# Performance work log

Measured on AMD Instinct MI355X. Metric: run time of the kernel, lower is better.

Reference implementation:

```python
import jax, jax.numpy as jnp
import numpy as np
import math

B, N, D, H = 4, 2048, 1024, 16
DH = D // H  # dim per head
OUT = 1024

def setup_inputs() -> dict:
    key0 = jax.random.key(0)
    ks = jax.random.split(key0, 12)
    s = 1.0 / math.sqrt(D)
    return {
        "key": jax.random.normal(ks[0], (B, N, D), jnp.float32),
        "value": jax.random.normal(ks[1], (B, N, D), jnp.float32),
        "query": jax.random.normal(ks[2], (B, N, D), jnp.float32),
        "Wk": jax.random.normal(ks[3], (D, D), jnp.float32) * s,
        "bk": jax.random.normal(ks[4], (D,), jnp.float32) * 0.01,
        "Wv": jax.random.normal(ks[5], (D, D), jnp.float32) * s,
        "bv": jax.random.normal(ks[6], (D,), jnp.float32) * 0.01,
        "Wq": jax.random.normal(ks[7], (D, D), jnp.float32) * s,
        "bq": jax.random.normal(ks[8], (D,), jnp.float32) * 0.01,
        "Wo": jax.random.normal(ks[9], (D, OUT), jnp.float32) * s,
        "bo": jax.random.normal(ks[10], (OUT,), jnp.float32) * 0.01,
    }

def reference(key, value, query, Wk, bk, Wv, bv, Wq, bq, Wo, bo):
    scale = math.sqrt(DH)
    k = (key @ Wk + bk).reshape(B, N, H, DH).transpose(0, 2, 1, 3)    # [B,H,N,DH]
    v = (value @ Wv + bv).reshape(B, N, H, DH).transpose(0, 2, 1, 3)
    q = ((query @ Wq + bq) / scale).reshape(B, N, H, DH).transpose(0, 2, 1, 3)
    scores = jnp.einsum('bhqd,bhkd->bhqk', q, k).astype(jnp.float32)  # [B,H,N,N]
    attn = jax.nn.softmax(scores, axis=-1).astype(q.dtype)
    # dropout p=0.0 (eval / identity)
    ctx = jnp.einsum('bhqk,bhkd->bhqd', attn, v)                      # [B,H,N,DH]
    ctx = ctx.transpose(0, 2, 1, 3).reshape(B, N, D)
    out = ctx @ Wo + bo                                               # [B,N,OUT]
    return out
```

## Files before the change

### kernel.cpp

```cpp
#include <hip/hip_runtime.h>
#include <hip/hip_bf16.h>
#include <stdint.h>

#define BB 4
#define NN 2048
#define DD 1024
#define HH 16
#define DHH 64
#define MM (BB*NN)

typedef unsigned short u16;
typedef unsigned int u32;
typedef __bf16 bf16x8_t __attribute__((ext_vector_type(8)));
typedef float f32x4_t __attribute__((ext_vector_type(4)));
typedef float f32x16_t __attribute__((ext_vector_type(16)));

__device__ inline u16 f2b(float f) {
    __hip_bfloat16 h = __float2bfloat16(f);
    return *(u16*)&h;
}

__device__ inline u32 pack2(float lo, float hi) {
    return (u32)f2b(lo) | ((u32)f2b(hi) << 16);
}

__device__ inline void gload16(const void* g, void* l) {
    __builtin_amdgcn_global_load_lds(
        (const __attribute__((address_space(1))) void*)g,
        (__attribute__((address_space(3))) void*)l, 16, 0, 0);
}

__global__ void cvt_kernel(const float* __restrict__ in, u16* __restrict__ out) {
    int i = (blockIdx.x * 256 + threadIdx.x) * 4;
    float4 v = *(const float4*)(in + i);
    ushort4 o;
    o.x = f2b(v.x); o.y = f2b(v.y); o.z = f2b(v.z); o.w = f2b(v.w);
    *(ushort4*)(out + i) = o;
}

__global__ void wtrans_kernel(const float* __restrict__ W0, const float* __restrict__ W1,
                              const float* __restrict__ W2, const float* __restrict__ W3,
                              u16* __restrict__ out_base) {
    int z = blockIdx.z;
    const float* W = (z == 0) ? W0 : (z == 1) ? W1 : (z == 2) ? W2 : W3;
    u16* o = out_base + (size_t)z * DD * DD;
    __shared__ float tile[64][65];
    int t = threadIdx.x;
    int r0 = t >> 6;
    int c = t & 63;
    int kb = blockIdx.x, nb = blockIdx.y;
#pragma unroll
    for (int i = 0; i < 16; ++i) {
        int r = i * 4 + r0;
        tile[r][c] = W[(size_t)(kb * 64 + r) * DD + nb * 64 + c];
    }
    __syncthreads();
#pragma unroll
    for (int i = 0; i < 16; ++i) {
        int r = i * 4 + r0;
        o[(size_t)(nb * 64 + r) * DD + kb * 64 + c] = f2b(tile[c][r]);
    }
}

__global__ void vtrans_kernel(const u16* __restrict__ in, u16* __restrict__ out) {
    __shared__ u16 tile[64][65];
    const int t = threadIdx.x;
    const int r0 = t >> 6;
    const int c = t & 63;
    const int nt = blockIdx.x;
    const int bh = blockIdx.y;
    const int b = bh >> 4, h = bh & 15;
    const u16* src = in + ((size_t)(b * 2048 + nt * 64)) * DD + h * 64;
#pragma unroll
    for (int i = 0; i < 16; ++i) {
        int r = i * 4 + r0;
        tile[r][c] = src[(size_t)r * DD + c];
    }
    __syncthreads();
    u16* dst = out + ((size_t)bh * 64) * NN + nt * 64;
#pragma unroll
    for (int i = 0; i < 16; ++i) {
        int r = i * 4 + r0;
        dst[(size_t)r * NN + c] = tile[c][r];
    }
}

template<int OUT_F32>
__global__ __launch_bounds__(256, 2)
void gemm_bt(const u16* __restrict__ A, const u16* __restrict__ Bt,
             const float* __restrict__ bias, void* __restrict__ Cout, float scale) {
    __shared__ u16 As[128 * 64];
    __shared__ u16 Bs[128 * 64];
    const int t = threadIdx.x;
    const int w = t >> 6, l = t & 63;
    const int wm = w >> 1, wn = w & 1;
    const int g = l >> 4, c = l & 15;
    const int bm = blockIdx.x, bn = blockIdx.y;

    const f32x4_t vzero = {0.f, 0.f, 0.f, 0.f};
    f32x4_t acc[4][4];
#pragma unroll
    for (int m = 0; m < 4; ++m)
#pragma unroll
        for (int n = 0; n < 4; ++n) acc[m][n] = vzero;

    const int srow = l >> 3;
    const int scol = ((l & 7) ^ srow) << 3;
    const int sa = (l & 7) << 4;

    for (int ks = 0; ks < 16; ++ks) {
#pragma unroll
        for (int i = 0; i < 4; ++i) {
            int chunk = w * 4 + i;
            int row = chunk * 8 + srow;
            const u16* ga = A + (size_t)(bm * 128 + row) * DD + ks * 64 + scol;
            gload16(ga, As + chunk * 512);
            const u16* gb = Bt + (size_t)(bn * 128 + row) * DD + ks * 64 + scol;
            gload16(gb, Bs + chunk * 512);
        }
        __syncthreads();

        bf16x8_t af[4][2], bfr[4][2];
#pragma unroll
        for (int m = 0; m < 4; ++m) {
            int rowa = wm * 64 + m * 16 + c;
#pragma unroll
            for (int kk = 0; kk < 2; ++kk)
                af[m][kk] = *(const bf16x8_t*)&As[rowa * 64 + (((kk * 64 + g * 16) ^ sa) >> 1)];
        }
#pragma unroll
        for (int n = 0; n < 4; ++n) {
            int rowb = wn * 64 + n * 16 + c;
#pragma unroll
            for (int kk = 0; kk < 2; ++kk)
                bfr[n][kk] = *(const bf16x8_t*)&Bs[rowb * 64 + (((kk * 64 + g * 16) ^ sa) >> 1)];
        }
#pragma unroll
        for (int kk = 0; kk < 2; ++kk)
#pragma unroll
            for (int m = 0; m < 4; ++m)
#pragma unroll
                for (int n = 0; n < 4; ++n)
                    acc[m][n] = __builtin_amdgcn_mfma_f32_16x16x32_bf16(
                        af[m][kk], bfr[n][kk], acc[m][n], 0, 0, 0);
        __syncthreads();
    }

#pragma unroll
    for (int n = 0; n < 4; ++n) {
        int col = bn * 128 + wn * 64 + n * 16 + c;
        float bv = bias[col];
#pragma unroll
        for (int m = 0; m < 4; ++m) {
            int row = bm * 128 + wm * 64 + m * 16 + g * 4;
#pragma unroll
            for (int j = 0; j < 4; ++j) {
                float v = (acc[m][n][j] + bv) * scale;
                if (OUT_F32)
                    ((float*)Cout)[(size_t)(row + j) * DD + col] = v;
                else
                    ((u16*)Cout)[(size_t)(row + j) * DD + col] = f2b(v);
            }
        }
    }
}

__global__ __launch_bounds__(256, 2)
void attn32_kernel(const u16* __restrict__ qb, const u16* __restrict__ kb,
                   const u16* __restrict__ vt, u16* __restrict__ ctx) {
    __shared__ u16 Kt[2][64 * 64];
    __shared__ u16 Vs[2][64 * 64];
    const int t = threadIdx.x;
    const int w = t >> 6, l = t & 63;
    const int hl = l >> 5, l31 = l & 31, l7 = l & 7, l3 = l >> 3;

    const int f = blockIdx.y * 16 + blockIdx.x;
    const int wg = (f & 7) * 128 + (f >> 3);
    const int qt = wg & 15, bh = wg >> 4;
    const int b = bh >> 4, h = bh & 15;
    const int hoff = h * DHH;
    const size_t kv0 = (size_t)b * NN;
    const size_t vt0 = (size_t)bh * DHH;

    const size_t qrow = (size_t)(b * NN + qt * 128 + w * 32 + l31);
    bf16x8_t qf[4];
#pragma unroll
    for (int dks = 0; dks < 4; ++dks)
        qf[dks] = *(const bf16x8_t*)&qb[qrow * DD + hoff + dks * 16 + hl * 8];

    f32x16_t accO[2];
#pragma unroll
    for (int dt = 0; dt < 2; ++dt)
#pragma unroll
        for (int r = 0; r < 16; ++r) accO[dt][r] = 0.f;
    float lacc[16];
#pragma unroll
    for (int r = 0; r < 16; ++r) lacc[r] = 0.f;

#define STAGE_K(kt_, buf_)                                                   \
    do {                                                                     \
        _Pragma("unroll")                                                    \
        for (int i_ = 0; i_ < 2; ++i_) {                                     \
            int ch_ = w + i_ * 4;                                            \
            int r_ = ch_ * 8 + l3;                                           \
            int rr_ = (r_ >> 2) & 3;                                         \
            int pr_ = (rr_ == 1 || rr_ == 2) ? (r_ ^ 12) : r_;               \
            gload16(kb + (kv0 + (kt_) * 64 + pr_) * DD + hoff +              \
                        ((l7 ^ l3) << 3),                                    \
                    &Kt[buf_][ch_ * 512]);                                   \
        }                                                                    \
    } while (0)
#define STAGE_V(kt_, buf_)                                                   \
    do {                                                                     \
        _Pragma("unroll")                                                    \
        for (int i_ = 0; i_ < 2; ++i_) {                                     \
            int ch_ = w + i_ * 4;                                            \
            int r_ = ch_ * 8 + l3;                                           \
            gload16(vt + (vt0 + r_) * NN + (kt_) * 64 + ((l7 ^ l3) << 3),    \
                    &Vs[buf_][ch_ * 512]);                                   \
        }                                                                    \
    } while (0)

    STAGE_K(0, 0);
    STAGE_V(0, 0);
    __syncthreads();

    for (int kt = 0; kt < NN / 64; ++kt) {
        const int cur = kt & 1;
        if (kt < NN / 64 - 1) {
            STAGE_K(kt + 1, cur ^ 1);
            STAGE_V(kt + 1, cur ^ 1);
        }

        const char* Kc = (const char*)Kt[cur];
        f32x16_t accS[2];
        __builtin_amdgcn_s_setprio(1);
#pragma unroll
        for (int kt32 = 0; kt32 < 2; ++kt32) {
#pragma unroll
            for (int r = 0; r < 16; ++r) accS[kt32][r] = 0.f;
#pragma unroll
            for (int dks = 0; dks < 4; ++dks) {
                bf16x8_t kf = *(const bf16x8_t*)(Kc + (kt32 * 32 + l31) * 128 +
                                                 ((dks * 32 + hl * 16) ^ (l7 << 4)));
                accS[kt32] = __builtin_amdgcn_mfma_f32_32x32x16_bf16(
                    kf, qf[dks], accS[kt32], 0, 0, 0);
            }
        }
        __builtin_amdgcn_s_setprio(0);

#pragma unroll
        for (int r = 0; r < 16; ++r) {
            float p0 = exp2f(accS[0][r]);
            float p1 = exp2f(accS[1][r]);
            accS[0][r] = p0;
            accS[1][r] = p1;
            lacc[r] += p0 + p1;
        }

        const char* Vc = (const char*)Vs[cur];
        __builtin_amdgcn_s_setprio(1);
#pragma unroll
        for (int pm = 0; pm < 4; ++pm) {
            const int kt32 = pm >> 1, half = pm & 1;
            union { u32 u[4]; bf16x8_t v; } pu;
#pragma unroll
            for (int j2 = 0; j2 < 4; ++j2)
                pu.u[j2] = pack2(accS[kt32][half * 8 + 2 * j2],
                                 accS[kt32][half * 8 + 2 * j2 + 1]);
#pragma unroll
            for (int dt = 0; dt < 2; ++dt) {
                bf16x8_t vf = *(const bf16x8_t*)(Vc + (dt * 32 + l31) * 128 +
                                                 ((pm * 32 + hl * 16) ^ (l7 << 4)));
                accO[dt] = __builtin_amdgcn_mfma_f32_32x32x16_bf16(
                    vf, pu.v, accO[dt], 0, 0, 0);
            }
        }
        __builtin_amdgcn_s_setprio(0);
        __syncthreads();
    }

    float rsum = 0.f;
#pragma unroll
    for (int r = 0; r < 16; ++r) rsum += lacc[r];
    rsum += __shfl_xor(rsum, 32);
    const float rl = 1.0f / rsum;
#pragma unroll
    for (int dt = 0; dt < 2; ++dt)
#pragma unroll
        for (int m = 0; m < 4; ++m) {
            ushort4 o;
            o.x = f2b(accO[dt][4 * m + 0] * rl);
            o.y = f2b(accO[dt][4 * m + 1] * rl);
            o.z = f2b(accO[dt][4 * m + 2] * rl);
            o.w = f2b(accO[dt][4 * m + 3] * rl);
            *(ushort4*)&ctx[qrow * DD + hoff + dt * 32 + m * 8 + hl * 4] = o;
        }
#undef STAGE_K
#undef STAGE_V
}

extern "C" void kernel_launch(void* const* d_in, const int* in_sizes, int n_in,
                              void* d_out, int out_size, void* d_ws, size_t ws_size,
                              hipStream_t stream) {
    (void)in_sizes; (void)n_in; (void)out_size; (void)ws_size;
    const float* key   = (const float*)d_in[0];
    const float* value = (const float*)d_in[1];
    const float* query = (const float*)d_in[2];
    const float* Wk = (const float*)d_in[3];
    const float* bk = (const float*)d_in[4];
    const float* Wv = (const float*)d_in[5];
    const float* bv = (const float*)d_in[6];
    const float* Wq = (const float*)d_in[7];
    const float* bq = (const float*)d_in[8];
    const float* Wo = (const float*)d_in[9];
    const float* bo = (const float*)d_in[10];

    char* ws = (char*)d_ws;
    const size_t MB = 1024 * 1024;
    u16* qbuf = (u16*)(ws + 0 * MB);
    u16* kbuf = (u16*)(ws + 16 * MB);
    u16* vbuf = (u16*)(ws + 32 * MB);
    u16* WtK  = (u16*)(ws + 48 * MB);
    u16* WtV  = (u16*)(ws + 50 * MB);
    u16* WtQ  = (u16*)(ws + 52 * MB);
    u16* WtO  = (u16*)(ws + 54 * MB);
    u16* xb   = (u16*)(ws + 56 * MB);

    const int nelem = MM * DD;
    const int cvt_blocks = nelem / (256 * 4);

    wtrans_kernel<<<dim3(16, 16, 4), 256, 0, stream>>>(Wk, Wv, Wq, Wo, WtK);

    cvt_kernel<<<cvt_blocks, 256, 0, stream>>>(value, xb);
    gemm_bt<0><<<dim3(64, 8), 256, 0, stream>>>(xb, WtV, bv, vbuf, 1.0f);
    cvt_kernel<<<cvt_blocks, 256, 0, stream>>>(key, xb);
    gemm_bt<0><<<dim3(64, 8), 256, 0, stream>>>(xb, WtK, bk, kbuf, 1.0f);
    cvt_kernel<<<cvt_blocks, 256, 0, stream>>>(query, xb);
    gemm_bt<0><<<dim3(64, 8), 256, 0, stream>>>(xb, WtQ, bq, qbuf, 0.125f * 1.4426950408889634f);

    u16* VT = xb;
    vtrans_kernel<<<dim3(32, 64), 256, 0, stream>>>(vbuf, VT);

    u16* ctx = vbuf;
    attn32_kernel<<<dim3(16, 64), 256, 0, stream>>>(qbuf, kbuf, VT, ctx);

    gemm_bt<1><<<dim3(64, 8), 256, 0, stream>>>(ctx, WtO, bo, d_out, 1.0f);
}
```

Before: 242.9 us.

## Give each attention wave two 32-row query tiles and halve block size

The attention kernel now launches 128-thread blocks in which each wave handles 64 query rows as two 32-row tiles. K and V fragments are loaded from shared memory once per tile and reused across both query tiles, which halves LDS reads per MFMA. Staging pointers are precomputed and advanced each iteration, the row-sum uses a tree reduction into one scalar per tile, and pack2 uses the paired bf16 conversion. The trade is higher register pressure from doubled accumulators and fewer waves per block to hide latency.

New measurement: 245.9 us. Within noise of the previous version (+1.2%).

```diff
diff --git a/kernel.cpp b/kernel.cpp
--- a/kernel.cpp
+++ b/kernel.cpp
@@ -21,7 +21,8 @@
 }
 
 __device__ inline u32 pack2(float lo, float hi) {
-    return (u32)f2b(lo) | ((u32)f2b(hi) << 16);
+    __hip_bfloat162 h2 = __float22bfloat162_rn(make_float2(lo, hi));
+    return *(u32*)&h2;
 }
 
 __device__ inline void gload16(const void* g, void* l) {
@@ -165,7 +166,7 @@
     }
 }
 
-__global__ __launch_bounds__(256, 2)
+__global__ __launch_bounds__(128, 2)
 void attn32_kernel(const u16* __restrict__ qb, const u16* __restrict__ kb,
                    const u16* __restrict__ vt, u16* __restrict__ ctx) {
     __shared__ u16 Kt[2][64 * 64];
@@ -182,122 +183,150 @@
     const size_t kv0 = (size_t)b * NN;
     const size_t vt0 = (size_t)bh * DHH;
 
-    const size_t qrow = (size_t)(b * NN + qt * 128 + w * 32 + l31);
-    bf16x8_t qf[4];
-#pragma unroll
-    for (int dks = 0; dks < 4; ++dks)
-        qf[dks] = *(const bf16x8_t*)&qb[qrow * DD + hoff + dks * 16 + hl * 8];
-
-    f32x16_t accO[2];
-#pragma unroll
-    for (int dt = 0; dt < 2; ++dt)
-#pragma unroll
-        for (int r = 0; r < 16; ++r) accO[dt][r] = 0.f;
-    float lacc[16];
-#pragma unroll
-    for (int r = 0; r < 16; ++r) lacc[r] = 0.f;
-
-#define STAGE_K(kt_, buf_)                                                   \
+    const size_t qrow_base = (size_t)(b * NN + qt * 128 + w * 64);
+    bf16x8_t qf[2][4];
+#pragma unroll
+    for (int qm = 0; qm < 2; ++qm)
+#pragma unroll
+        for (int dks = 0; dks < 4; ++dks)
+            qf[qm][dks] = *(const bf16x8_t*)&qb[(qrow_base + qm * 32 + l31) * DD +
+                                                hoff + dks * 16 + hl * 8];
+
+    f32x16_t accO[2][2];
+#pragma unroll
+    for (int qm = 0; qm < 2; ++qm)
+#pragma unroll
+        for (int dt = 0; dt < 2; ++dt)
+#pragma unroll
+            for (int r = 0; r < 16; ++r) accO[qm][dt][r] = 0.f;
+    float lacc[2] = {0.f, 0.f};
+
+    const int scol2 = (l7 ^ l3) << 3;
+    const u16* kp[4];
+    const u16* vp[4];
+#pragma unroll
+    for (int i = 0; i < 4; ++i) {
+        const int ch = w * 4 + i, r = ch * 8 + l3, rr = (r >> 2) & 3;
+        const int pr = (rr == 1 || rr == 2) ? (r ^ 12) : r;
+        kp[i] = kb + (kv0 + pr) * DD + hoff + scol2;
+        vp[i] = vt + (vt0 + r) * NN + scol2;
+    }
+
+#define STAGE(buf_)                                                          \
     do {                                                                     \
         _Pragma("unroll")                                                    \
-        for (int i_ = 0; i_ < 2; ++i_) {                                     \
-            int ch_ = w + i_ * 4;                                            \
-            int r_ = ch_ * 8 + l3;                                           \
-            int rr_ = (r_ >> 2) & 3;                                         \
-            int pr_ = (rr_ == 1 || rr_ == 2) ? (r_ ^ 12) : r_;               \
-            gload16(kb + (kv0 + (kt_) * 64 + pr_) * DD + hoff +              \
-                        ((l7 ^ l3) << 3),                                    \
-                    &Kt[buf_][ch_ * 512]);                                   \
+        for (int i_ = 0; i_ < 4; ++i_) {                                     \
+            gload16(kp[i_], &Kt[buf_][(w * 4 + i_) * 512]);                  \
+            gload16(vp[i_], &Vs[buf_][(w * 4 + i_) * 512]);                  \
         }                                                                    \
     } while (0)
-#define STAGE_V(kt_, buf_)                                                   \
+#define ADV()                                                                \
     do {                                                                     \
         _Pragma("unroll")                                                    \
-        for (int i_ = 0; i_ < 2; ++i_) {                                     \
-            int ch_ = w + i_ * 4;                                            \
-            int r_ = ch_ * 8 + l3;                                           \
-            gload16(vt + (vt0 + r_) * NN + (kt_) * 64 + ((l7 ^ l3) << 3),    \
-                    &Vs[buf_][ch_ * 512]);                                   \
-        }                                                                    \
+        for (int i_ = 0; i_ < 4; ++i_) { kp[i_] += 64 * DD; vp[i_] += 64; }  \
     } while (0)
 
-    STAGE_K(0, 0);
-    STAGE_V(0, 0);
+    STAGE(0);
+    ADV();
     __syncthreads();
 
     for (int kt = 0; kt < NN / 64; ++kt) {
         const int cur = kt & 1;
         if (kt < NN / 64 - 1) {
-            STAGE_K(kt + 1, cur ^ 1);
-            STAGE_V(kt + 1, cur ^ 1);
-        }
-
+            STAGE(cur ^ 1);
+            ADV();
+        }
         const char* Kc = (const char*)Kt[cur];
-        f32x16_t accS[2];
+        const char* Vc = (const char*)Vs[cur];
+
+        bf16x8_t kf[2][4];
+#pragma unroll
+        for (int kt32 = 0; kt32 < 2; ++kt32)
+#pragma unroll
+            for (int dks = 0; dks < 4; ++dks)
+                kf[kt32][dks] = *(const bf16x8_t*)(Kc + (kt32 * 32 + l31) * 128 +
+                                                   ((dks * 32 + hl * 16) ^ (l7 << 4)));
+
+        f32x16_t accS[2][2];
         __builtin_amdgcn_s_setprio(1);
 #pragma unroll
-        for (int kt32 = 0; kt32 < 2; ++kt32) {
-#pragma unroll
-            for (int r = 0; r < 16; ++r) accS[kt32][r] = 0.f;
-#pragma unroll
-            for (int dks = 0; dks < 4; ++dks) {
-                bf16x8_t kf = *(const bf16x8_t*)(Kc + (kt32 * 32 + l31) * 128 +
-                                                 ((dks * 32 + hl * 16) ^ (l7 << 4)));
-                accS[kt32] = __builtin_amdgcn_mfma_f32_32x32x16_bf16(
-                    kf, qf[dks], accS[kt32], 0, 0, 0);
+        for (int qm = 0; qm < 2; ++qm)
+#pragma unroll
+            for (int kt32 = 0; kt32 < 2; ++kt32) {
+#pragma unroll
+                for (int r = 0; r < 16; ++r) accS[qm][kt32][r] = 0.f;
+#pragma unroll
+                for (int dks = 0; dks < 4; ++dks)
+                    accS[qm][kt32] = __builtin_amdgcn_mfma_f32_32x32x16_bf16(
+                        kf[kt32][dks], qf[qm][dks], accS[qm][kt32], 0, 0, 0);
             }
-        }
         __builtin_amdgcn_s_setprio(0);
 
 #pragma unroll
-        for (int r = 0; r < 16; ++r) {
-            float p0 = exp2f(accS[0][r]);
-            float p1 = exp2f(accS[1][r]);
-            accS[0][r] = p0;
-            accS[1][r] = p1;
-            lacc[r] += p0 + p1;
-        }
-
-        const char* Vc = (const char*)Vs[cur];
+        for (int qm = 0; qm < 2; ++qm) {
+#pragma unroll
+            for (int kt32 = 0; kt32 < 2; ++kt32)
+#pragma unroll
+                for (int r = 0; r < 16; ++r)
+                    accS[qm][kt32][r] = exp2f(accS[qm][kt32][r]);
+            f32x16_t sv = accS[qm][0] + accS[qm][1];
+            float s8[8];
+#pragma unroll
+            for (int r = 0; r < 8; ++r) s8[r] = sv[r] + sv[r + 8];
+#pragma unroll
+            for (int sl = 4; sl >= 1; sl >>= 1)
+#pragma unroll
+                for (int r = 0; r < sl; ++r) s8[r] += s8[r + sl];
+            lacc[qm] += s8[0];
+        }
+
+        bf16x8_t vf[4][2];
+#pragma unroll
+        for (int pm = 0; pm < 4; ++pm)
+#pragma unroll
+            for (int dt = 0; dt < 2; ++dt)
+                vf[pm][dt] = *(const bf16x8_t*)(Vc + (dt * 32 + l31) * 128 +
+                                                ((pm * 32 + hl * 16) ^ (l7 << 4)));
+
         __builtin_amdgcn_s_setprio(1);
 #pragma unroll
-        for (int pm = 0; pm < 4; ++pm) {
-            const int kt32 = pm >> 1, half = pm & 1;
-            union { u32 u[4]; bf16x8_t v; } pu;
-#pragma unroll
-            for (int j2 = 0; j2 < 4; ++j2)
-                pu.u[j2] = pack2(accS[kt32][half * 8 + 2 * j2],
-                                 accS[kt32][half * 8 + 2 * j2 + 1]);
-#pragma unroll
-            for (int dt = 0; dt < 2; ++dt) {
-                bf16x8_t vf = *(const bf16x8_t*)(Vc + (dt * 32 + l31) * 128 +
-                                                 ((pm * 32 + hl * 16) ^ (l7 << 4)));
-                accO[dt] = __builtin_amdgcn_mfma_f32_32x32x16_bf16(
-                    vf, pu.v, accO[dt], 0, 0, 0);
+        for (int qm = 0; qm < 2; ++qm)
+#pragma unroll
+            for (int pm = 0; pm < 4; ++pm) {
+                const int kt32 = pm >> 1, half = pm & 1;
+                union { u32 u[4]; bf16x8_t v; } pu;
+#pragma unroll
+                for (int j2 = 0; j2 < 4; ++j2)
+                    pu.u[j2] = pack2(accS[qm][kt32][half * 8 + 2 * j2],
+                                     accS[qm][kt32][half * 8 + 2 * j2 + 1]);
+#pragma unroll
+                for (int dt = 0; dt < 2; ++dt)
+                    accO[qm][dt] = __builtin_amdgcn_mfma_f32_32x32x16_bf16(
+                        vf[pm][dt], pu.v, accO[qm][dt], 0, 0, 0);
             }
-        }
         __builtin_amdgcn_s_setprio(0);
         __syncthreads();
     }
-
-    float rsum = 0.f;
-#pragma unroll
-    for (int r = 0; r < 16; ++r) rsum += lacc[r];
-    rsum += __shfl_xor(rsum, 32);
-    const float rl = 1.0f / rsum;
-#pragma unroll
-    for (int dt = 0; dt < 2; ++dt)
-#pragma unroll
-        for (int m = 0; m < 4; ++m) {
-            ushort4 o;
-            o.x = f2b(accO[dt][4 * m + 0] * rl);
-            o.y = f2b(accO[dt][4 * m + 1] * rl);
-            o.z = f2b(accO[dt][4 * m + 2] * rl);
-            o.w = f2b(accO[dt][4 * m + 3] * rl);
-            *(ushort4*)&ctx[qrow * DD + hoff + dt * 32 + m * 8 + hl * 4] = o;
-        }
-#undef STAGE_K
-#undef STAGE_V
+#undef STAGE
+#undef ADV
+
+#pragma unroll
+    for (int qm = 0; qm < 2; ++qm) {
+        float rsum = lacc[qm] + __shfl_xor(lacc[qm], 32);
+        const float rl = 1.0f / rsum;
+        const size_t qrow = qrow_base + qm * 32 + l31;
+#pragma unroll
+        for (int dt = 0; dt < 2; ++dt)
+#pragma unroll
+            for (int m = 0; m < 4; ++m) {
+                ushort4 o;
+                o.x = f2b(accO[qm][dt][4 * m + 0] * rl);
+                o.y = f2b(accO[qm][dt][4 * m + 1] * rl);
+                o.z = f2b(accO[qm][dt][4 * m + 2] * rl);
+                o.w = f2b(accO[qm][dt][4 * m + 3] * rl);
+                *(ushort4*)&ctx[qrow * DD + hoff + dt * 32 + m * 8 + hl * 4] = o;
+            }
+    }
 }
 
 extern "C" void kernel_launch(void* const* d_in, const int* in_sizes, int n_in,
@@ -343,7 +372,7 @@
     vtrans_kernel<<<dim3(32, 64), 256, 0, stream>>>(vbuf, VT);
 
     u16* ctx = vbuf;
-    attn32_kernel<<<dim3(16, 64), 256, 0, stream>>>(qbuf, kbuf, VT, ctx);
+    attn32_kernel<<<dim3(16, 64), 128, 0, stream>>>(qbuf, kbuf, VT, ctx);
 
     gemm_bt<1><<<dim3(64, 8), 256, 0, stream>>>(ctx, WtO, bo, d_out, 1.0f);
 }
```
